# Optimization experiments

Measured on AMD Instinct MI355X. Metric: run time of the kernel, lower is better.

Reference implementation:

```python
import jax, jax.numpy as jnp
import numpy as np

D_MODEL = 512
D_STATE = 64
D_INNER = 2 * D_MODEL   # standard Mamba expand=2
D_CONV = 4
DT_RANK = D_MODEL // 16  # 32
LN_EPS = 1e-5


def setup_inputs() -> dict:
    key = jax.random.key(0)
    ks = jax.random.split(key, 12)
    B, L = 2, 1024
    s = 0.02
    return {
        "frames": jax.random.normal(ks[0], (B, L, D_MODEL), jnp.float32),
        "gamma": jnp.ones((D_MODEL,), jnp.float32),
        "beta": jnp.zeros((D_MODEL,), jnp.float32),
        "W_in": jax.random.normal(ks[1], (D_MODEL, 2 * D_INNER), jnp.float32) * s,
        "conv_w": jax.random.normal(ks[2], (D_INNER, D_CONV), jnp.float32) * s,
        "conv_b": jnp.zeros((D_INNER,), jnp.float32),
        "W_x": jax.random.normal(ks[3], (D_INNER, DT_RANK + 2 * D_STATE), jnp.float32) * s,
        "W_dt": jax.random.normal(ks[4], (DT_RANK, D_INNER), jnp.float32) * s,
        "b_dt": jax.random.uniform(ks[5], (D_INNER,), jnp.float32, -4.0, -2.0),
        "A_log": jnp.log(jnp.broadcast_to(jnp.arange(1, D_STATE + 1, dtype=jnp.float32), (D_INNER, D_STATE))),
        "D": jnp.ones((D_INNER,), jnp.float32),
        "W_out": jax.random.normal(ks[6], (D_INNER, D_MODEL), jnp.float32) * s,
    }


def reference(frames, gamma, beta, W_in, conv_w, conv_b, W_x, W_dt, b_dt, A_log, D, W_out):
    B, L, _ = frames.shape
    d_inner = W_in.shape[1] // 2
    d_state = A_log.shape[1]
    dt_rank = W_dt.shape[0]
    d_conv = conv_w.shape[1]

    # LayerNorm
    mu = frames.mean(-1, keepdims=True)
    var = ((frames - mu) ** 2).mean(-1, keepdims=True)
    xn = (frames - mu) * jax.lax.rsqrt(var + LN_EPS) * gamma + beta

    # in_proj -> x, z
    x, z = jnp.split(xn @ W_in, 2, axis=-1)  # each (B, L, d_inner)

    # causal depthwise conv1d along time
    xc = jnp.pad(x.transpose(0, 2, 1), ((0, 0), (0, 0), (d_conv - 1, 0)))  # (B, d_inner, L+pad)
    xconv = jax.lax.conv_general_dilated(
        xc, conv_w[:, None, :], (1,), "VALID", feature_group_count=d_inner)  # (B, d_inner, L)
    x = jax.nn.silu(xconv.transpose(0, 2, 1) + conv_b)  # (B, L, d_inner)

    # input-dependent dt, B, C
    xdb = x @ W_x
    dt, Bm, Cm = jnp.split(xdb, [dt_rank, dt_rank + d_state], axis=-1)
    delta = jax.nn.softplus(dt @ W_dt + b_dt)  # (B, L, d_inner)
    A = -jnp.exp(A_log)                        # (d_inner, d_state)

    # selective scan over time
    def step(h, inp):
        d_t, B_t, C_t, x_t = inp  # (B,d_inner) (B,d_state) (B,d_state) (B,d_inner)
        dA = jnp.exp(d_t[..., None] * A)                       # (B,d_inner,d_state)
        h = h * dA + (d_t * x_t)[..., None] * B_t[:, None, :]  # (B,d_inner,d_state)
        y = jnp.einsum("bds,bs->bd", h, C_t)
        return h, y

    h0 = jnp.zeros((B, d_inner, d_state), frames.dtype)
    xs = (delta.transpose(1, 0, 2), Bm.transpose(1, 0, 2),
          Cm.transpose(1, 0, 2), x.transpose(1, 0, 2))
    _, ys = jax.lax.scan(step, h0, xs)  # (L, B, d_inner)

    y = ys.transpose(1, 0, 2) + x * D
    y = y * jax.nn.silu(z)
    return y @ W_out + frames  # residual connection
```

## Files before the change

kernel.cpp:

```cpp
#include <hip/hip_runtime.h>
#include <hip/hip_bf16.h>
#include <math.h>

constexpr int Bn     = 2;
constexpr int Lseq   = 1024;
constexpr int DM     = 512;
constexpr int DI     = 1024;
constexpr int DS     = 64;
constexpr int RNK    = 32;
constexpr int NROWS  = Bn * Lseq;
constexpr int XDBW   = RNK + 2 * DS;
constexpr int CH     = 64;
constexpr int NC     = Lseq / CH;
constexpr int DROWS  = 8;

constexpr float LOG2E = 1.44269504088896340736f;

typedef __attribute__((ext_vector_type(4))) float floatx4;
typedef __attribute__((ext_vector_type(8))) short shortx8;

__device__ __forceinline__ float silu_f(float v) {
    return v / (1.f + __expf(-v));
}

__device__ __forceinline__ float rdl(float v, int l) {
    return __int_as_float(__builtin_amdgcn_readlane(__float_as_int(v), l));
}

__device__ __forceinline__ float bf2f(unsigned short u) {
    return __uint_as_float((unsigned)u << 16);
}

__device__ __forceinline__ float exp2_fast(float x) {
#if __has_builtin(__builtin_amdgcn_exp2f)
    return __builtin_amdgcn_exp2f(x);
#else
    return exp2f(x);
#endif
}

__global__ void prep_kernel(const float* __restrict__ x, const float* __restrict__ g,
                            const float* __restrict__ be,
                            const float* __restrict__ Wi, const float* __restrict__ Wo,
                            const float* __restrict__ Wx,
                            __hip_bfloat16* __restrict__ xn,
                            __hip_bfloat16* __restrict__ Ti, __hip_bfloat16* __restrict__ To,
                            __hip_bfloat16* __restrict__ Tx) {
    __shared__ float tile[64][65];
    __shared__ float red[8];
    int bid = blockIdx.x;
    int tid = threadIdx.x;
    if (bid < NROWS) {
        int row = bid;
        const float* xr = x + (size_t)row * DM;
        float v0 = xr[tid], v1 = xr[tid + 256];
        float s = v0 + v1, sq = v0 * v0 + v1 * v1;
        #pragma unroll
        for (int o = 1; o < 64; o <<= 1) {
            s  += __shfl_xor(s, o);
            sq += __shfl_xor(sq, o);
        }
        int w = tid >> 6;
        if ((tid & 63) == 0) { red[w] = s; red[4 + w] = sq; }
        __syncthreads();
        float ts = red[0] + red[1] + red[2] + red[3];
        float tq = red[4] + red[5] + red[6] + red[7];
        float mu  = ts * (1.f / DM);
        float var = tq * (1.f / DM) - mu * mu;
        float inv = rsqrtf(var + 1e-5f);
        __hip_bfloat16* o0 = xn + (size_t)row * DM;
        o0[tid]       = __float2bfloat16((v0 - mu) * inv * g[tid]       + be[tid]);
        o0[tid + 256] = __float2bfloat16((v1 - mu) * inv * g[tid + 256] + be[tid + 256]);
        return;
    }
    int b2 = bid - NROWS;
    const float* in; __hip_bfloat16* out; int R, Cc, bx, by;
    if (b2 < 256)      { in = Wi; out = Ti; R = DM; Cc = 2 * DI; bx = b2 & 31; by = b2 >> 5; }
    else if (b2 < 384) { int b3 = b2 - 256; in = Wo; out = To; R = DI; Cc = DM;   bx = b3 & 7; by = b3 >> 3; }
    else               { int b3 = b2 - 384; in = Wx; out = Tx; R = DI; Cc = XDBW; bx = b3 % 3; by = b3 / 3; }
    int r0 = by * 64, c0 = bx * 64;
    #pragma unroll
    for (int i = tid; i < 4096; i += 256) {
        int r = i >> 6, c = i & 63;
        tile[r][c] = (r0 + r < R && c0 + c < Cc) ? in[(size_t)(r0 + r) * Cc + c0 + c] : 0.f;
    }
    __syncthreads();
    #pragma unroll
    for (int i = tid; i < 4096; i += 256) {
        int c = i >> 6, r = i & 63;
        if (r0 + r < R && c0 + c < Cc)
            out[(size_t)(c0 + c) * R + r0 + r] = __float2bfloat16(tile[r][c]);
    }
}

__global__ __launch_bounds__(512) void gemm_inproj(const __hip_bfloat16* __restrict__ A,
                                                   const __hip_bfloat16* __restrict__ Bt,
                                                   __hip_bfloat16* __restrict__ xh,
                                                   __hip_bfloat16* __restrict__ zh,
                                                   int M, int N, int K) {
    __shared__ __hip_bfloat16 As[128 * 64];
    __shared__ __hip_bfloat16 Bs[128 * 64];
    const int tid  = threadIdx.x;
    const int wave = tid >> 6, lane = tid & 63;
    const int m0 = blockIdx.y * 128, n0 = blockIdx.x * 128;
    const int wm = (wave >> 2) * 64, wn = (wave & 3) * 32;

    floatx4 acc[4][2] = {};

    const int arow16 = lane & 15;
    const int kgrp   = lane >> 4;

    for (int k0 = 0; k0 < K; k0 += 64) {
        #pragma unroll
        for (int p = 0; p < 2; ++p) {
            int j = tid + p * 512;
            int h = j >> 9, rs = j & 511;
            int row = rs >> 2, seg = rs & 3;
            const __hip_bfloat16* gA = A  + (size_t)(m0 + row) * K + k0 + h * 32 + seg * 8;
            const __hip_bfloat16* gB = Bt + (size_t)(n0 + row) * K + k0 + h * 32 + seg * 8;
            __hip_bfloat16* lA = As + (size_t)(wave * 64 + p * 512) * 8;
            __hip_bfloat16* lB = Bs + (size_t)(wave * 64 + p * 512) * 8;
            __builtin_amdgcn_global_load_lds(
                (const __attribute__((address_space(1))) void*)gA,
                (__attribute__((address_space(3))) void*)lA, 16, 0, 0);
            __builtin_amdgcn_global_load_lds(
                (const __attribute__((address_space(1))) void*)gB,
                (__attribute__((address_space(3))) void*)lB, 16, 0, 0);
        }
        __syncthreads();

        const shortx8* Asv = (const shortx8*)As;
        const shortx8* Bsv = (const shortx8*)Bs;
        #pragma unroll
        for (int h = 0; h < 2; ++h) {
            shortx8 a[4], b[2];
            #pragma unroll
            for (int i = 0; i < 4; ++i)
                a[i] = Asv[h * 512 + (wm + i * 16 + arow16) * 4 + kgrp];
            #pragma unroll
            for (int j = 0; j < 2; ++j)
                b[j] = Bsv[h * 512 + (wn + j * 16 + arow16) * 4 + kgrp];
            #pragma unroll
            for (int i = 0; i < 4; ++i)
                #pragma unroll
                for (int j = 0; j < 2; ++j)
                    acc[i][j] = __builtin_amdgcn_mfma_f32_16x16x32_bf16(a[i], b[j], acc[i][j], 0, 0, 0);
        }
        __syncthreads();
    }

    const int drow = (lane >> 4) * 4;
    const int dcol = lane & 15;
    const bool isz = (n0 >= DI);
    __hip_bfloat16* dst = isz ? zh : xh;
    const int coloff = isz ? DI : 0;
    #pragma unroll
    for (int i = 0; i < 4; ++i)
        #pragma unroll
        for (int j = 0; j < 2; ++j) {
            int rowb = m0 + wm + i * 16 + drow;
            int col  = n0 + wn + j * 16 + dcol - coloff;
            #pragma unroll
            for (int r = 0; r < 4; ++r)
                dst[(size_t)(rowb + r) * DI + col] = __float2bfloat16(acc[i][j][r]);
        }
}

template<bool RES>
__global__ __launch_bounds__(512) void gemm64_sk(const __hip_bfloat16* __restrict__ A,
                                                 const __hip_bfloat16* __restrict__ Bt,
                                                 const float* __restrict__ Res,
                                                 float* __restrict__ C,
                                                 int M, int N, int K) {
    __shared__ __hip_bfloat16 As[2][64 * 64];
    __shared__ __hip_bfloat16 Bs[2][64 * 64];
    __shared__ float red[256 * 17];
    const int tid  = threadIdx.x;
    const int wave = tid >> 6, lane = tid & 63;
    const int g = wave >> 2, w2 = wave & 3;
    const int m0 = blockIdx.y * 64, n0 = blockIdx.x * 64;
    const int wm = (w2 >> 1) * 32, wn = (w2 & 1) * 32;

    floatx4 acc[2][2] = {};

    const int arow16 = lane & 15;
    const int kgrp   = lane >> 4;
    const int kbeg   = g * (K / 2);

    for (int kk = 0; kk < K / 2; kk += 64) {
        int k0 = kbeg + kk;
        #pragma unroll
        for (int p = 0; p < 2; ++p) {
            int j = (w2 * 64 + lane) + p * 256;
            int h = j >> 8, rs = j & 255;
            int row = rs >> 2, seg = rs & 3;
            int brow = n0 + row; if (brow >= N) brow = N - 1;
            const __hip_bfloat16* gA = A  + (size_t)(m0 + row) * K + k0 + h * 32 + seg * 8;
            const __hip_bfloat16* gB = Bt + (size_t)brow * K + k0 + h * 32 + seg * 8;
            __hip_bfloat16* lA = As[g] + (size_t)(w2 * 64 + p * 256) * 8;
            __hip_bfloat16* lB = Bs[g] + (size_t)(w2 * 64 + p * 256) * 8;
            __builtin_amdgcn_global_load_lds(
                (const __attribute__((address_space(1))) void*)gA,
                (__attribute__((address_space(3))) void*)lA, 16, 0, 0);
            __builtin_amdgcn_global_load_lds(
                (const __attribute__((address_space(1))) void*)gB,
                (__attribute__((address_space(3))) void*)lB, 16, 0, 0);
        }
        __syncthreads();

        const shortx8* Asv = (const shortx8*)As[g];
        const shortx8* Bsv = (const shortx8*)Bs[g];
        #pragma unroll
        for (int h = 0; h < 2; ++h) {
            shortx8 a[2], b[2];
            #pragma unroll
            for (int i = 0; i < 2; ++i)
                a[i] = Asv[h * 256 + (wm + i * 16 + arow16) * 4 + kgrp];
            #pragma unroll
            for (int j = 0; j < 2; ++j)
                b[j] = Bsv[h * 256 + (wn + j * 16 + arow16) * 4 + kgrp];
            #pragma unroll
            for (int i = 0; i < 2; ++i)
                #pragma unroll
                for (int j = 0; j < 2; ++j)
                    acc[i][j] = __builtin_amdgcn_mfma_f32_16x16x32_bf16(a[i], b[j], acc[i][j], 0, 0, 0);
        }
        __syncthreads();
    }

    int rbase = (w2 * 64 + lane) * 17;
    if (g == 1) {
        #pragma unroll
        for (int i = 0; i < 2; ++i)
            #pragma unroll
            for (int j = 0; j < 2; ++j)
                *(float4*)&red[rbase + (i * 2 + j) * 4] =
                    make_float4(acc[i][j][0], acc[i][j][1], acc[i][j][2], acc[i][j][3]);
    }
    __syncthreads();
    if (g == 0) {
        const int drow = (lane >> 4) * 4;
        const int dcol = lane & 15;
        #pragma unroll
        for (int i = 0; i < 2; ++i)
            #pragma unroll
            for (int j = 0; j < 2; ++j) {
                float4 part = *(const float4*)&red[rbase + (i * 2 + j) * 4];
                int rowb = m0 + wm + i * 16 + drow;
                int col  = n0 + wn + j * 16 + dcol;
                if (col < N) {
                    #pragma unroll
                    for (int r = 0; r < 4; ++r) {
                        size_t idx = (size_t)(rowb + r) * N + col;
                        float v = acc[i][j][r] + (&part.x)[r];
                        if (RES) v += Res[idx];
                        C[idx] = v;
                    }
                }
            }
    }
}

__global__ __launch_bounds__(256) void conv_tile(const __hip_bfloat16* __restrict__ xh,
                                                 const __hip_bfloat16* __restrict__ zh,
                                                 const float* __restrict__ cw,
                                                 const float* __restrict__ cb,
                                                 __hip_bfloat16* __restrict__ xcv_bf,
                                                 __hip_bfloat16* __restrict__ xcvT,
                                                 __hip_bfloat16* __restrict__ zgT) {
    __shared__ float xt[67][68];
    __shared__ float tb[64][65];
    __shared__ float tb2[64][65];
    int t0 = blockIdx.x * 64, d0 = blockIdx.y * 64, b = blockIdx.z;
    int tid = threadIdx.x;
    size_t rowbase = (size_t)b * Lseq;

    for (int i = tid; i < 67 * 16; i += 256) {
        int r = i >> 4, j = i & 15;
        int t = t0 - 3 + r;
        float4 v4 = make_float4(0.f, 0.f, 0.f, 0.f);
        if (t >= 0) {
            ushort4 u = *(const ushort4*)&xh[(rowbase + t) * DI + d0 + j * 4];
            v4 = make_float4(bf2f(u.x), bf2f(u.y), bf2f(u.z), bf2f(u.w));
        }
        *(float4*)&xt[r][j * 4] = v4;
    }
    for (int i = tid; i < 64 * 16; i += 256) {
        int r = i >> 4, j = i & 15;
        ushort4 u = *(const ushort4*)&zh[(rowbase + t0 + r) * DI + d0 + j * 4];
        tb2[r][j * 4 + 0] = silu_f(bf2f(u.x));
        tb2[r][j * 4 + 1] = silu_f(bf2f(u.y));
        tb2[r][j * 4 + 2] = silu_f(bf2f(u.z));
        tb2[r][j * 4 + 3] = silu_f(bf2f(u.w));
    }
    __syncthreads();

    {
        int d = tid & 63, tg = tid >> 6;
        float4 cwv = *(const float4*)&cw[(d0 + d) * 4];
        float cbv = cb[d0 + d];
        #pragma unroll
        for (int i = 0; i < 16; ++i) {
            int t = tg * 16 + i;
            float acc = cbv;
            #pragma unroll
            for (int k = 0; k < 4; ++k) acc += xt[t + k][d] * (&cwv.x)[k];
            float v = silu_f(acc);
            tb[t][d] = v;
            xcv_bf[(rowbase + t0 + t) * DI + d0 + d] = __float2bfloat16(v);
        }
    }
    __syncthreads();

    {
        int t2 = tid & 63, dg2 = tid >> 6;
        #pragma unroll
        for (int i = 0; i < 16; ++i) {
            int d = dg2 * 16 + i;
            size_t orow = ((size_t)(b * DI + d0 + d)) * Lseq + t0 + t2;
            xcvT[orow] = __float2bfloat16(tb[t2][d]);
            zgT[orow]  = __float2bfloat16(tb2[t2][d]);
        }
    }
}

__global__ __launch_bounds__(256) void delta_kernel(const float* __restrict__ xdb,
                                                    const float* __restrict__ Wdt,
                                                    const float* __restrict__ bdt,
                                                    float* __restrict__ delta) {
    int r0 = blockIdx.y * DROWS;
    int d = blockIdx.x * 256 + threadIdx.x;
    __shared__ float dtv[RNK][DROWS];
    if (threadIdx.x < DROWS * RNK) {
        int k = threadIdx.x >> 5, r = threadIdx.x & 31;
        dtv[r][k] = xdb[(size_t)(r0 + k) * XDBW + r];
    }
    __syncthreads();
    float bb = bdt[d];
    float acc[DROWS];
    #pragma unroll
    for (int k = 0; k < DROWS; ++k) acc[k] = bb;
    #pragma unroll
    for (int r = 0; r < RNK; ++r) {
        float wv = Wdt[(size_t)r * DI + d];
        float4 lo = *(const float4*)&dtv[r][0];
        float4 hi = *(const float4*)&dtv[r][4];
        acc[0] += lo.x * wv; acc[1] += lo.y * wv;
        acc[2] += lo.z * wv; acc[3] += lo.w * wv;
        acc[4] += hi.x * wv; acc[5] += hi.y * wv;
        acc[6] += hi.z * wv; acc[7] += hi.w * wv;
    }
    #pragma unroll
    for (int k = 0; k < DROWS; ++k) {
        float a = acc[k];
        float sp = (a > 20.f) ? a : log1pf(__expf(a));
        delta[(size_t)(r0 + k) * DI + d] = sp;
    }
}

__global__ __launch_bounds__(512) void scan_full(
        const float* __restrict__ delta, const __hip_bfloat16* __restrict__ xcvT,
        const float* __restrict__ xdb, const __hip_bfloat16* __restrict__ zgT,
        const float* __restrict__ A_log, const float* __restrict__ Dp,
        __hip_bfloat16* __restrict__ y_row) {
    __shared__ float Bsh[2][64][65];
    __shared__ float Csh[2][64][65];
    __shared__ float dsh[2][64][9];
    __shared__ float P[8][8 * 65];
    __shared__ float T[64 * 9];

    int blk = blockIdx.x;
    int dg  = blk & 127;
    int b   = blk >> 7;
    int tid = threadIdx.x, w = tid >> 6, lane = tid & 63;
    int d = dg * 8 + w;

    float a2 = -__expf(A_log[d * DS + lane]) * LOG2E;
    float Dv = Dp[d];

    const int st_t = tid >> 3, st_d = tid & 7;

    {
        int r0 = b * Lseq;
        #pragma unroll
        for (int k = 0; k < 2; ++k) {
            int i = tid + k * 512;
            int t = i >> 4, sg = i & 15;
            const float* rowp = &xdb[(size_t)(r0 + t) * XDBW + RNK];
            *(float4*)&Bsh[0][t][sg * 4] = *(const float4*)&rowp[sg * 4];
            *(float4*)&Csh[0][t][sg * 4] = *(const float4*)&rowp[DS + sg * 4];
        }
        dsh[0][st_t][st_d] = delta[(size_t)(r0 + st_t) * DI + dg * 8 + st_d];
    }
    __syncthreads();

    const unsigned short* xT = (const unsigned short*)xcvT;
    const unsigned short* zT = (const unsigned short*)zgT;
    const size_t chbase = (size_t)(b * DI + d) * Lseq;

    float xv = bf2f(xT[chbase + lane]);
    float zv = bf2f(zT[chbase + lane]);

    float h = 0.f;
    float* Pw = P[w];
    const int tr = lane & 7, q = lane >> 3;
    const int rdbase = tr * 65 + q * 8;

    for (int c = 0; c < NC; ++c) {
        int cur = c & 1;

        float4 pb0, pc0, pb1, pc1;
        float pd = 0.f, nxv = 0.f, nzv = 0.f;
        if (c + 1 < NC) {
            int r1 = b * Lseq + (c + 1) * CH;
            {
                int t = tid >> 4, sg = tid & 15;
                const float* rowp = &xdb[(size_t)(r1 + t) * XDBW + RNK];
                pb0 = *(const float4*)&rowp[sg * 4];
                pc0 = *(const float4*)&rowp[DS + sg * 4];
            }
            {
                int i = tid + 512;
                int t = i >> 4, sg = i & 15;
                const float* rowp = &xdb[(size_t)(r1 + t) * XDBW + RNK];
                pb1 = *(const float4*)&rowp[sg * 4];
                pc1 = *(const float4*)&rowp[DS + sg * 4];
            }
            pd  = delta[(size_t)(r1 + st_t) * DI + dg * 8 + st_d];
            nxv = bf2f(xT[chbase + (c + 1) * CH + lane]);
            nzv = bf2f(zT[chbase + (c + 1) * CH + lane]);
        }

        int r0 = b * Lseq + c * CH;
        float vd  = dsh[cur][lane][w];
        float vpx = vd * xv;
        float y = 0.f;

        #pragma unroll
        for (int t8 = 0; t8 < 8; ++t8) {
            #pragma unroll
            for (int tt = 0; tt < 8; ++tt) {
                int t = t8 * 8 + tt;
                float Bt = Bsh[cur][t][lane];
                float Ct = Csh[cur][t][lane];
                h = h * exp2_fast(rdl(vd, t) * a2) + rdl(vpx, t) * Bt;
                Pw[tt * 65 + lane] = h * Ct;
            }
            float sacc = 0.f;
            #pragma unroll
            for (int j = 0; j < 8; ++j) sacc += Pw[rdbase + j];
            sacc += __shfl_xor(sacc, 8);
            sacc += __shfl_xor(sacc, 16);
            sacc += __shfl_xor(sacc, 32);
            if (q == t8) y = sacc;
        }

        float yv = (y + xv * Dv) * zv;

        __syncthreads();
        T[lane * 9 + w] = yv;
        if (c + 1 < NC) {
            int nxt = cur ^ 1;
            {
                int t = tid >> 4, sg = tid & 15;
                *(float4*)&Bsh[nxt][t][sg * 4] = pb0;
                *(float4*)&Csh[nxt][t][sg * 4] = pc0;
            }
            {
                int i = tid + 512;
                int t = i >> 4, sg = i & 15;
                *(float4*)&Bsh[nxt][t][sg * 4] = pb1;
                *(float4*)&Csh[nxt][t][sg * 4] = pc1;
            }
            dsh[nxt][st_t][st_d] = pd;
        }
        __syncthreads();

        {
            float v = T[st_t * 9 + st_d];
            y_row[(size_t)(r0 + st_t) * DI + dg * 8 + st_d] = __float2bfloat16(v);
        }

        xv = nxv; zv = nzv;
    }
}

extern "C" void kernel_launch(void* const* d_in, const int* in_sizes, int n_in,
                              void* d_out, int out_size, void* d_ws, size_t ws_size,
                              hipStream_t stream) {
    const float* frames = (const float*)d_in[0];
    const float* gamma  = (const float*)d_in[1];
    const float* beta   = (const float*)d_in[2];
    const float* W_in   = (const float*)d_in[3];
    const float* conv_w = (const float*)d_in[4];
    const float* conv_b = (const float*)d_in[5];
    const float* W_x    = (const float*)d_in[6];
    const float* W_dt   = (const float*)d_in[7];
    const float* b_dt   = (const float*)d_in[8];
    const float* A_log  = (const float*)d_in[9];
    const float* Dp     = (const float*)d_in[10];
    const float* W_out  = (const float*)d_in[11];
    float* out = (float*)d_out;

    char* ws = (char*)d_ws;
    __hip_bfloat16* xn_bf  = (__hip_bfloat16*)ws; ws += (size_t)NROWS * DM * 2;
    __hip_bfloat16* Wt_in  = (__hip_bfloat16*)ws; ws += (size_t)(2 * DI) * DM * 2;
    __hip_bfloat16* Wt_out = (__hip_bfloat16*)ws; ws += (size_t)DM * DI * 2;
    __hip_bfloat16* Wt_x   = (__hip_bfloat16*)ws; ws += (size_t)XDBW * DI * 2;
    __hip_bfloat16* y_row  = (__hip_bfloat16*)ws; ws += (size_t)NROWS * DI * 2;
    __hip_bfloat16* xcv_bf = (__hip_bfloat16*)ws; ws += (size_t)NROWS * DI * 2;
    __hip_bfloat16* xh     = (__hip_bfloat16*)ws; ws += (size_t)NROWS * DI * 2;
    __hip_bfloat16* zh     = (__hip_bfloat16*)ws; ws += (size_t)NROWS * DI * 2;
    __hip_bfloat16* xcvT   = (__hip_bfloat16*)ws; ws += (size_t)NROWS * DI * 2;
    __hip_bfloat16* zgT    = (__hip_bfloat16*)ws; ws += (size_t)NROWS * DI * 2;
    float* xdb    = (float*)ws;  ws += (size_t)NROWS * XDBW * 4;
    float* delta  = (float*)ws;  ws += (size_t)NROWS * DI * 4;

    prep_kernel<<<NROWS + 432, 256, 0, stream>>>(frames, gamma, beta, W_in, W_out, W_x,
                                                 xn_bf, Wt_in, Wt_out, Wt_x);

    gemm_inproj<<<dim3(2 * DI / 128, NROWS / 128), 512, 0, stream>>>(
        xn_bf, Wt_in, xh, zh, NROWS, 2 * DI, DM);

    conv_tile<<<dim3(Lseq / 64, DI / 64, Bn), 256, 0, stream>>>(
        xh, zh, conv_w, conv_b, xcv_bf, xcvT, zgT);

    gemm64_sk<false><<<dim3((XDBW + 63) / 64, NROWS / 64), 512, 0, stream>>>(
        xcv_bf, Wt_x, nullptr, xdb, NROWS, XDBW, DI);

    delta_kernel<<<dim3(DI / 256, NROWS / DROWS), 256, 0, stream>>>(xdb, W_dt, b_dt, delta);

    scan_full<<<Bn * (DI / 8), 512, 0, stream>>>(delta, xcvT, xdb, zgT, A_log, Dp, y_row);

    gemm64_sk<true><<<dim3(DM / 64, NROWS / 64), 512, 0, stream>>>(
        y_row, Wt_out, frames, out, NROWS, DM, DI);
}
```

Measured before the change: 220.7 us.

## Transpose B/C chunks in LDS and preload all delta in scan kernel

Stores B and C chunk tiles transposed in shared memory so each lane can read eight consecutive time steps with vector loads instead of scalar per-step loads. The delta values for the whole sequence and channel group are loaded into shared memory once up front, which removes the per-chunk delta prefetch. Partial-product reads also switch to float4. This adds a larger LDS footprint (the full-length delta buffer) and scattered transposed stores, which may cut occupancy or cause bank conflicts.

```diff
diff --git a/kernel.cpp b/kernel.cpp
--- a/kernel.cpp
+++ b/kernel.cpp
@@ -363,10 +363,10 @@
         const float* __restrict__ xdb, const __hip_bfloat16* __restrict__ zgT,
         const float* __restrict__ A_log, const float* __restrict__ Dp,
         __hip_bfloat16* __restrict__ y_row) {
-    __shared__ float Bsh[2][64][65];
-    __shared__ float Csh[2][64][65];
-    __shared__ float dsh[2][64][9];
-    __shared__ float P[8][8 * 65];
+    __shared__ float BT[2][64][68];
+    __shared__ float CT[2][64][68];
+    __shared__ float dall[Lseq][9];
+    __shared__ float P[8][8 * 68];
     __shared__ float T[64 * 9];
 
     int blk = blockIdx.x;
@@ -380,17 +380,24 @@
 
     const int st_t = tid >> 3, st_d = tid & 7;
 
-    {
-        int r0 = b * Lseq;
-        #pragma unroll
-        for (int k = 0; k < 2; ++k) {
-            int i = tid + k * 512;
-            int t = i >> 4, sg = i & 15;
-            const float* rowp = &xdb[(size_t)(r0 + t) * XDBW + RNK];
-            *(float4*)&Bsh[0][t][sg * 4] = *(const float4*)&rowp[sg * 4];
-            *(float4*)&Csh[0][t][sg * 4] = *(const float4*)&rowp[DS + sg * 4];
-        }
-        dsh[0][st_t][st_d] = delta[(size_t)(r0 + st_t) * DI + dg * 8 + st_d];
+    #pragma unroll
+    for (int k = 0; k < 16; ++k) {
+        int i = tid + k * 512;
+        int t = i >> 3, ch = i & 7;
+        dall[t][ch] = delta[(size_t)(b * Lseq + t) * DI + dg * 8 + ch];
+    }
+    #pragma unroll
+    for (int k = 0; k < 2; ++k) {
+        int i = tid + k * 512;
+        int t = i >> 4, sg = i & 15;
+        const float* rowp = &xdb[(size_t)(b * Lseq + t) * XDBW + RNK];
+        float4 bv = *(const float4*)&rowp[sg * 4];
+        float4 cv = *(const float4*)&rowp[DS + sg * 4];
+        #pragma unroll
+        for (int j = 0; j < 4; ++j) {
+            BT[0][4 * sg + j][t] = (&bv.x)[j];
+            CT[0][4 * sg + j][t] = (&cv.x)[j];
+        }
     }
     __syncthreads();
 
@@ -402,15 +409,15 @@
     float zv = bf2f(zT[chbase + lane]);
 
     float h = 0.f;
-    float* Pw = P[w];
+    float* Pw = (float*)P[w];
     const int tr = lane & 7, q = lane >> 3;
-    const int rdbase = tr * 65 + q * 8;
+    const int rdbase = tr * 68 + q * 8;
 
     for (int c = 0; c < NC; ++c) {
         int cur = c & 1;
 
         float4 pb0, pc0, pb1, pc1;
-        float pd = 0.f, nxv = 0.f, nzv = 0.f;
+        float nxv = 0.f, nzv = 0.f;
         if (c + 1 < NC) {
             int r1 = b * Lseq + (c + 1) * CH;
             {
@@ -426,29 +433,33 @@
                 pb1 = *(const float4*)&rowp[sg * 4];
                 pc1 = *(const float4*)&rowp[DS + sg * 4];
             }
-            pd  = delta[(size_t)(r1 + st_t) * DI + dg * 8 + st_d];
             nxv = bf2f(xT[chbase + (c + 1) * CH + lane]);
             nzv = bf2f(zT[chbase + (c + 1) * CH + lane]);
         }
 
-        int r0 = b * Lseq + c * CH;
-        float vd  = dsh[cur][lane][w];
+        float vd  = dall[(c << 6) + lane][w];
         float vpx = vd * xv;
         float y = 0.f;
+        const float* Bt = &BT[cur][lane][0];
+        const float* Ct = &CT[cur][lane][0];
 
         #pragma unroll
         for (int t8 = 0; t8 < 8; ++t8) {
+            float4 b0 = *(const float4*)&Bt[t8 * 8];
+            float4 b1 = *(const float4*)&Bt[t8 * 8 + 4];
+            float4 c0 = *(const float4*)&Ct[t8 * 8];
+            float4 c1 = *(const float4*)&Ct[t8 * 8 + 4];
             #pragma unroll
             for (int tt = 0; tt < 8; ++tt) {
                 int t = t8 * 8 + tt;
-                float Bt = Bsh[cur][t][lane];
-                float Ct = Csh[cur][t][lane];
-                h = h * exp2_fast(rdl(vd, t) * a2) + rdl(vpx, t) * Bt;
-                Pw[tt * 65 + lane] = h * Ct;
+                float Bv = (tt < 4) ? (&b0.x)[tt] : (&b1.x)[tt - 4];
+                float Cv = (tt < 4) ? (&c0.x)[tt] : (&c1.x)[tt - 4];
+                h = h * exp2_fast(rdl(vd, t) * a2) + rdl(vpx, t) * Bv;
+                Pw[tt * 68 + lane] = h * Cv;
             }
-            float sacc = 0.f;
-            #pragma unroll
-            for (int j = 0; j < 8; ++j) sacc += Pw[rdbase + j];
+            float4 ra = *(const float4*)&Pw[rdbase];
+            float4 rb = *(const float4*)&Pw[rdbase + 4];
+            float sacc = ra.x + ra.y + ra.z + ra.w + rb.x + rb.y + rb.z + rb.w;
             sacc += __shfl_xor(sacc, 8);
             sacc += __shfl_xor(sacc, 16);
             sacc += __shfl_xor(sacc, 32);
@@ -463,22 +474,27 @@
             int nxt = cur ^ 1;
             {
                 int t = tid >> 4, sg = tid & 15;
-                *(float4*)&Bsh[nxt][t][sg * 4] = pb0;
-                *(float4*)&Csh[nxt][t][sg * 4] = pc0;
+                #pragma unroll
+                for (int j = 0; j < 4; ++j) {
+                    BT[nxt][4 * sg + j][t] = (&pb0.x)[j];
+                    CT[nxt][4 * sg + j][t] = (&pc0.x)[j];
+                }
             }
             {
                 int i = tid + 512;
                 int t = i >> 4, sg = i & 15;
-                *(float4*)&Bsh[nxt][t][sg * 4] = pb1;
-                *(float4*)&Csh[nxt][t][sg * 4] = pc1;
+                #pragma unroll
+                for (int j = 0; j < 4; ++j) {
+                    BT[nxt][4 * sg + j][t] = (&pb1.x)[j];
+                    CT[nxt][4 * sg + j][t] = (&pc1.x)[j];
+                }
             }
-            dsh[nxt][st_t][st_d] = pd;
         }
         __syncthreads();
 
         {
             float v = T[st_t * 9 + st_d];
-            y_row[(size_t)(r0 + st_t) * DI + dg * 8 + st_d] = __float2bfloat16(v);
+            y_row[(size_t)(b * Lseq + c * CH + st_t) * DI + dg * 8 + st_d] = __float2bfloat16(v);
         }
 
         xv = nxv; zv = nzv;
```

New measurement: 242.8 us. +10.0%, slower.
